# Performance work log

Measured on AMD Instinct MI355X. Metric: run time of the kernel, lower is better.

The kernel has to match this reference:

```python
import jax, jax.numpy as jnp
import numpy as np

N_EMBED = 256
N_HEADS = 4
HEAD_SIZE = N_EMBED // N_HEADS  # 64
BLOCK_SIZE = 768
LN_EPS = 1e-5


def layer_norm(x, g, b):
    mu = jnp.mean(x, axis=-1, keepdims=True)
    var = jnp.var(x, axis=-1, keepdims=True)
    return (x - mu) * jax.lax.rsqrt(var + LN_EPS) * g + b


def setup_inputs() -> dict:
    key = jax.random.key(0)
    ks = jax.random.split(key, 12)
    B, T, C, H, hs = 32, BLOCK_SIZE, N_EMBED, N_HEADS, HEAD_SIZE
    s_in = 1.0 / np.sqrt(C)
    s_ff = 1.0 / np.sqrt(4 * C)
    return {
        "x": jax.random.normal(ks[0], (B, T, C), jnp.float32),
        # per-head projections, stacked: [H, C, hs]
        "Wq": jax.random.normal(ks[1], (H, C, hs), jnp.float32) * s_in,
        "Wk": jax.random.normal(ks[2], (H, C, hs), jnp.float32) * s_in,
        "Wv": jax.random.normal(ks[3], (H, C, hs), jnp.float32) * s_in,
        "Wo": jax.random.normal(ks[4], (C, C), jnp.float32) * s_in,
        "bo": jnp.zeros((C,), jnp.float32),
        "W1": jax.random.normal(ks[5], (C, 4 * C), jnp.float32) * s_in,
        "b1": jnp.zeros((4 * C,), jnp.float32),
        "W2": jax.random.normal(ks[6], (4 * C, C), jnp.float32) * s_ff,
        "b2": jnp.zeros((C,), jnp.float32),
        "g1": jnp.ones((C,), jnp.float32),
        "be1": jnp.zeros((C,), jnp.float32),
        "g2": jnp.ones((C,), jnp.float32),
        "be2": jnp.zeros((C,), jnp.float32),
    }


def reference(x, Wq, Wk, Wv, Wo, bo, W1, b1, W2, b2, g1, be1, g2, be2):
    B, T, C = x.shape
    # --- multi-head causal self-attention (pre-LN) ---
    h = layer_norm(x, g1, be1)
    q = jnp.einsum("btc,hcd->bhtd", h, Wq)
    k = jnp.einsum("btc,hcd->bhtd", h, Wk)
    v = jnp.einsum("btc,hcd->bhtd", h, Wv)
    scores = jnp.einsum("bhtd,bhsd->bhts", q, k) * (HEAD_SIZE ** -0.5)
    causal = jnp.tril(jnp.ones((T, T), bool))
    scores = jnp.where(causal, scores, -jnp.inf)
    attn = jax.nn.softmax(scores, axis=-1)  # dropout = identity (eval)
    o = jnp.einsum("bhts,bhsd->bhtd", attn, v)
    o = o.transpose(0, 2, 1, 3).reshape(B, T, C)  # concat heads
    x = x + o @ Wo + bo
    # --- feed-forward (pre-LN) ---
    h2 = layer_norm(x, g2, be2)
    x = x + jax.nn.relu(h2 @ W1 + b1) @ W2 + b2
    return x
```

## Files before the change

kernel.cpp:

```cpp
#include <hip/hip_runtime.h>
#include <stdint.h>

using short8   = __attribute__((ext_vector_type(8))) short;
using f32x4    = __attribute__((ext_vector_type(4))) float;
using ushort4v = __attribute__((ext_vector_type(4))) unsigned short;
using uint2v   = __attribute__((ext_vector_type(2))) unsigned int;

#define CSC  0.1803368801111f
#define FIXC 20.0f

__device__ __forceinline__ unsigned short f2bf(float f) {
    unsigned int u = __builtin_bit_cast(unsigned int, f);
    u += 0x7FFFu + ((u >> 16) & 1u);
    return (unsigned short)(u >> 16);
}
__device__ __forceinline__ float bf2f(unsigned short s) {
    unsigned int u = ((unsigned int)s) << 16;
    return __builtin_bit_cast(float, u);
}
__device__ __forceinline__ unsigned pk2bf(float a, float b) {
    unsigned r;
    asm("v_cvt_pk_bf16_f32 %0, %1, %2" : "=v"(r) : "v"(a), "v"(b));
    return r;
}

__device__ __forceinline__ void gload16(const void* g, void* l) {
    __builtin_amdgcn_global_load_lds(
        (const __attribute__((address_space(1))) void*)(uintptr_t)g,
        (__attribute__((address_space(3))) void*)(unsigned)(uintptr_t)l,
        16, 0, 0);
}

__device__ __forceinline__ uint2v ln_row_pk(f32x4 v, f32x4 gv, f32x4 bvv) {
    float s  = v[0] + v[1] + v[2] + v[3];
    float s2 = v[0]*v[0] + v[1]*v[1] + v[2]*v[2] + v[3]*v[3];
    for (int m = 1; m < 64; m <<= 1) {
        s  += __shfl_xor(s,  m, 64);
        s2 += __shfl_xor(s2, m, 64);
    }
    float mu  = s * (1.0f / 256.0f);
    float var = s2 * (1.0f / 256.0f) - mu * mu;
    float rs  = rsqrtf(var + 1e-5f);
    float r0 = (v[0] - mu) * rs * gv[0] + bvv[0];
    float r1 = (v[1] - mu) * rs * gv[1] + bvv[1];
    float r2 = (v[2] - mu) * rs * gv[2] + bvv[2];
    float r3 = (v[3] - mu) * rs * gv[3] + bvv[3];
    uint2v u; u[0] = pk2bf(r0, r1); u[1] = pk2bf(r2, r3);
    return u;
}

__global__ __launch_bounds__(256) void prep_k(const float* __restrict__ x, const float* __restrict__ g1,
                                              const float* __restrict__ be1, unsigned short* __restrict__ h,
                                              const float* __restrict__ Wq, const float* __restrict__ Wk,
                                              const float* __restrict__ Wv, const float* __restrict__ Wo,
                                              const float* __restrict__ W1, const float* __restrict__ W2,
                                              unsigned short* __restrict__ wpackT, unsigned short* __restrict__ woT,
                                              unsigned short* __restrict__ w1T, unsigned short* __restrict__ w2T) {
    __shared__ float t[64][65];
    if (blockIdx.x >= 192) {
        int row  = (blockIdx.x - 192) * 4 + (threadIdx.x >> 6);
        int lane = threadIdx.x & 63;
        f32x4 v = *(const f32x4*)(x + (size_t)row * 256 + lane * 4);
        f32x4 gv = *(const f32x4*)(g1 + lane * 4);
        f32x4 bv = *(const f32x4*)(be1 + lane * 4);
        uint2v u = ln_row_pk(v, gv, bv);
        *(uint2v*)(h + (size_t)row * 256 + lane * 4) = u;
        return;
    }
    const int bid = blockIdx.x;
    const float* in; unsigned short* out;
    int R, C, r0, c0;
    if (bid < 48) {
        int z = bid >> 2, cx = bid & 3;
        int qkv = z >> 2, hh = z & 3;
        in = ((qkv == 0) ? Wq : (qkv == 1) ? Wk : Wv) + (size_t)hh * 256 * 64;
        out = wpackT + (size_t)(qkv * 256 + hh * 64) * 256;
        R = 256; C = 64; r0 = cx * 64; c0 = 0;
    } else if (bid < 64) {
        int tt = bid - 48;
        in = Wo; out = woT; R = 256; C = 256; r0 = (tt >> 2) * 64; c0 = (tt & 3) * 64;
    } else if (bid < 128) {
        int tt = bid - 64;
        in = W1; out = w1T; R = 256; C = 1024; r0 = (tt & 3) * 64; c0 = (tt >> 2) * 64;
    } else {
        int tt = bid - 128;
        in = W2; out = w2T; R = 1024; C = 256; r0 = (tt & 15) * 64; c0 = (tt >> 4) * 64;
    }
    const int tx = threadIdx.x & 63, ty = threadIdx.x >> 6;
    #pragma unroll
    for (int i = 0; i < 64; i += 4)
        t[i + ty][tx] = in[(size_t)(r0 + i + ty) * C + c0 + tx];
    __syncthreads();
    #pragma unroll
    for (int i = 0; i < 64; i += 4)
        out[(size_t)(c0 + i + ty) * R + r0 + tx] = f2bf(t[tx][i + ty]);
}

__global__ __launch_bounds__(256) void qkv_k(const unsigned short* __restrict__ h,
                                             const unsigned short* __restrict__ wpackT,
                                             unsigned short* __restrict__ qk,
                                             unsigned short* __restrict__ vT) {
    __shared__ unsigned short As[128 * 64];
    __shared__ unsigned short Bs[128 * 64];
    const int tid  = threadIdx.x;
    const int lane = tid & 63;
    const int w    = tid >> 6;
    const int wm   = w >> 1, wn = w & 1;
    const int l15  = lane & 15, l4 = lane >> 4;
    const int bid  = blockIdx.x;

    const unsigned short *A, *BT;
    unsigned short* outp;
    int bm, bn, N;
    float qsc = 1.0f;
    if (bid < 768) {
        bn = bid & 3;  bm = bid >> 2;
        A = h; BT = wpackT; outp = qk; N = 512;
        if (bn < 2) qsc = CSC;
    } else {
        int t = bid - 768;
        bm = t & 1;    bn = t >> 1;
        A = wpackT + 512 * 256; BT = h; outp = vT; N = 24576;
    }
    const int K = 256;

    f32x4 acc[4][4] = {};

    const size_t K2 = (size_t)K * 2;
    const int i0   = w * 4096 + lane * 16;
    const int row0 = i0 >> 7;
    const int cb0  = (i0 & 127) ^ ((row0 & 7) << 4);
    const char* aSrc = (const char*)A  + ((size_t)(bm * 128 + row0)) * K2 + cb0;
    const char* bSrc = (const char*)BT + ((size_t)(bn * 128 + row0)) * K2 + cb0;

    for (int t = 0; t < 4; ++t) {
        {
            const char* aS = aSrc + (size_t)t * 128;
            const char* bS = bSrc + (size_t)t * 128;
            char* aD = (char*)&As[0] + w * 4096;
            char* bD = (char*)&Bs[0] + w * 4096;
            #pragma unroll
            for (int c = 0; c < 4; ++c) {
                gload16(aS + (size_t)c * 8 * K2, aD + c * 1024);
                gload16(bS + (size_t)c * 8 * K2, bD + c * 1024);
            }
        }
        __syncthreads();
        #pragma unroll
        for (int kf = 0; kf < 2; ++kf) {
            int kb = kf * 64 + l4 * 16;
            short8 af[4], bfr[4];
            #pragma unroll
            for (int mf = 0; mf < 4; ++mf) {
                int row = wm * 64 + mf * 16 + l15;
                af[mf] = *(const short8*)((const char*)&As[0] + ((row * 128 + kb) ^ ((row & 7) << 4)));
            }
            #pragma unroll
            for (int nf = 0; nf < 4; ++nf) {
                int row = wn * 64 + nf * 16 + l15;
                bfr[nf] = *(const short8*)((const char*)&Bs[0] + ((row * 128 + kb) ^ ((row & 7) << 4)));
            }
            #pragma unroll
            for (int mf = 0; mf < 4; ++mf)
                #pragma unroll
                for (int nf = 0; nf < 4; ++nf)
                    acc[mf][nf] = __builtin_amdgcn_mfma_f32_16x16x32_bf16(af[mf], bfr[nf], acc[mf][nf], 0, 0, 0);
        }
        __syncthreads();
    }

    #pragma unroll
    for (int nf = 0; nf < 4; ++nf) {
        int col = bn * 128 + wn * 64 + nf * 16 + l15;
        #pragma unroll
        for (int mf = 0; mf < 4; ++mf) {
            int row0o = bm * 128 + wm * 64 + mf * 16 + l4 * 4;
            size_t off = (size_t)row0o * N + col;
            unsigned p01 = pk2bf(acc[mf][nf][0] * qsc, acc[mf][nf][1] * qsc);
            unsigned p23 = pk2bf(acc[mf][nf][2] * qsc, acc[mf][nf][3] * qsc);
            outp[off]                 = (unsigned short)p01;
            outp[off + (size_t)N]     = (unsigned short)(p01 >> 16);
            outp[off + (size_t)N * 2] = (unsigned short)p23;
            outp[off + (size_t)N * 3] = (unsigned short)(p23 >> 16);
        }
    }
}

template <int EPI, bool DB>
__global__ __launch_bounds__(256) void gemm_bt(const unsigned short* __restrict__ A,
                                               const unsigned short* __restrict__ BT,
                                               void* __restrict__ outp,
                                               const float* __restrict__ bias,
                                               const void* __restrict__ resid,
                                               int K, int N) {
    __shared__ unsigned short As[DB ? 2 : 1][128 * 64];
    __shared__ unsigned short Bs[DB ? 2 : 1][128 * 64];
    const int tid  = threadIdx.x;
    const int lane = tid & 63;
    const int w    = tid >> 6;
    const int wm   = w >> 1, wn = w & 1;
    const int bm   = blockIdx.y, bn = blockIdx.x;
    const int l15  = lane & 15, l4 = lane >> 4;

    f32x4 acc[4][4] = {};

    const size_t K2 = (size_t)K * 2;
    const int i0   = w * 4096 + lane * 16;
    const int row0 = i0 >> 7;
    const int cb0  = (i0 & 127) ^ ((row0 & 7) << 4);
    const char* aSrc = (const char*)A  + ((size_t)(bm * 128 + row0)) * K2 + cb0;
    const char* bSrc = (const char*)BT + ((size_t)(bn * 128 + row0)) * K2 + cb0;
    const int nt = K >> 6;

    auto stage = [&](int t, int buf) {
        const char* aS = aSrc + (size_t)t * 128;
        const char* bS = bSrc + (size_t)t * 128;
        char* aD = (char*)&As[buf][0] + w * 4096;
        char* bD = (char*)&Bs[buf][0] + w * 4096;
        #pragma unroll
        for (int c = 0; c < 4; ++c) {
            gload16(aS + (size_t)c * 8 * K2, aD + c * 1024);
            gload16(bS + (size_t)c * 8 * K2, bD + c * 1024);
        }
    };
    auto compute = [&](int buf) {
        const char* AsB = (const char*)&As[buf][0];
        const char* BsB = (const char*)&Bs[buf][0];
        #pragma unroll
        for (int kf = 0; kf < 2; ++kf) {
            int kb = kf * 64 + l4 * 16;
            short8 af[4], bfr[4];
            #pragma unroll
            for (int mf = 0; mf < 4; ++mf) {
                int row = wm * 64 + mf * 16 + l15;
                af[mf] = *(const short8*)(AsB + ((row * 128 + kb) ^ ((row & 7) << 4)));
            }
            #pragma unroll
            for (int nf = 0; nf < 4; ++nf) {
                int row = wn * 64 + nf * 16 + l15;
                bfr[nf] = *(const short8*)(BsB + ((row * 128 + kb) ^ ((row & 7) << 4)));
            }
            #pragma unroll
            for (int mf = 0; mf < 4; ++mf)
                #pragma unroll
                for (int nf = 0; nf < 4; ++nf)
                    acc[mf][nf] = __builtin_amdgcn_mfma_f32_16x16x32_bf16(af[mf], bfr[nf], acc[mf][nf], 0, 0, 0);
        }
    };

    if (DB) {
        stage(0, 0);
        for (int t = 0; t < nt; ++t) {
            const int cur = t & 1;
            __syncthreads();
            if (t + 1 < nt) stage(t + 1, cur ^ 1);
            compute(cur);
        }
    } else {
        for (int t = 0; t < nt; ++t) {
            stage(t, 0);
            __syncthreads();
            compute(0);
            __syncthreads();
        }
    }

    #pragma unroll
    for (int nf = 0; nf < 4; ++nf) {
        int col = bn * 128 + wn * 64 + nf * 16 + l15;
        float bv = bias[col];
        #pragma unroll
        for (int mf = 0; mf < 4; ++mf) {
            int row0o = bm * 128 + wm * 64 + mf * 16 + l4 * 4;
            size_t off = (size_t)row0o * N + col;
            float v[4];
            #pragma unroll
            for (int r = 0; r < 4; ++r)
                v[r] = acc[mf][nf][r] + bv + ((const float*)resid)[off + (size_t)r * N];
            unsigned short* O = (unsigned short*)outp;
            unsigned p01 = pk2bf(v[0], v[1]), p23 = pk2bf(v[2], v[3]);
            O[off]                 = (unsigned short)p01;
            O[off + (size_t)N]     = (unsigned short)(p01 >> 16);
            O[off + (size_t)N * 2] = (unsigned short)p23;
            O[off + (size_t)N * 3] = (unsigned short)(p23 >> 16);
        }
    }
}

__global__ __launch_bounds__(256) void ff_fused(const unsigned short* __restrict__ x1b,
                                                const float* __restrict__ g2,
                                                const float* __restrict__ be2,
                                                const unsigned short* __restrict__ w1T,
                                                const unsigned short* __restrict__ w2T,
                                                const float* __restrict__ b1,
                                                const float* __restrict__ b2,
                                                float* __restrict__ out) {
    __shared__ unsigned short sA[4][32 * 64];
    __shared__ unsigned short sW[16384];
    __shared__ unsigned short sAct[32 * 64];
    const int tid = threadIdx.x, lane = tid & 63, w = tid >> 6;
    const int l15 = lane & 15, l4 = lane >> 4;
    const int wm = w >> 1, wn = w & 1;
    const int r0 = blockIdx.x * 32;

    {
        f32x4 gv = *(const f32x4*)(g2 + lane * 4);
        f32x4 bv = *(const f32x4*)(be2 + lane * 4);
        const int ks = lane >> 4, colb = (lane & 15) * 8;
        #pragma unroll
        for (int it = 0; it < 8; ++it) {
            int row = it * 4 + w;
            ushort4v u4 = *(const ushort4v*)(x1b + (size_t)(r0 + row) * 256 + lane * 4);
            f32x4 v;
            #pragma unroll
            for (int i = 0; i < 4; ++i) v[i] = bf2f(u4[i]);
            uint2v u = ln_row_pk(v, gv, bv);
            *(uint2v*)((char*)&sA[0][0] + ks * 4096 + row * 128 + (colb ^ ((row & 7) << 4))) = u;
        }
    }

    f32x4 oacc[8] = {};

    for (int c = 0; c < 16; ++c) {
        {
            const char* wb = (const char*)w1T + (size_t)(c * 64) * 512;
            #pragma unroll
            for (int g = 0; g < 8; ++g) {
                int j = g * 4096 + tid * 16;
                int ks = j >> 13, row = (j >> 7) & 63, cb = j & 127;
                gload16(wb + (size_t)row * 512 + ks * 128 + (cb ^ ((row & 7) << 4)),
                        (char*)&sW[0] + j);
            }
        }
        __syncthreads();

        f32x4 aacc[2] = {};
        __builtin_amdgcn_s_setprio(1);
        #pragma unroll
        for (int ks = 0; ks < 4; ++ks) {
            #pragma unroll
            for (int kf = 0; kf < 2; ++kf) {
                const int kb = kf * 64 + l4 * 16;
                int hrow = wm * 16 + l15;
                short8 hf = *(const short8*)((const char*)&sA[ks][0] + ((hrow * 128 + kb) ^ ((hrow & 7) << 4)));
                #pragma unroll
                for (int nf = 0; nf < 2; ++nf) {
                    int row = wn * 32 + nf * 16 + l15;
                    short8 wf = *(const short8*)((const char*)&sW[ks * 4096] + ((row * 128 + kb) ^ ((row & 7) << 4)));
                    aacc[nf] = __builtin_amdgcn_mfma_f32_16x16x32_bf16(wf, hf, aacc[nf], 0, 0, 0);
                }
            }
        }
        __builtin_amdgcn_s_setprio(0);
        #pragma unroll
        for (int nf = 0; nf < 2; ++nf) {
            int nl = wn * 32 + nf * 16 + l4 * 4;
            f32x4 bv = *(const f32x4*)(b1 + c * 64 + nl);
            float v0 = aacc[nf][0] + bv[0]; v0 = v0 > 0.0f ? v0 : 0.0f;
            float v1 = aacc[nf][1] + bv[1]; v1 = v1 > 0.0f ? v1 : 0.0f;
            float v2 = aacc[nf][2] + bv[2]; v2 = v2 > 0.0f ? v2 : 0.0f;
            float v3 = aacc[nf][3] + bv[3]; v3 = v3 > 0.0f ? v3 : 0.0f;
            uint2v u; u[0] = pk2bf(v0, v1); u[1] = pk2bf(v2, v3);
            int m = wm * 16 + l15;
            *(uint2v*)((char*)&sAct[0] + ((m * 128 + nl * 2) ^ ((m & 7) << 4))) = u;
        }
        __syncthreads();

        {
            const char* wb = (const char*)w2T + (size_t)c * 128;
            #pragma unroll
            for (int g = 0; g < 8; ++g) {
                int j = g * 4096 + tid * 16;
                int row = j >> 7, cb = j & 127;
                gload16(wb + (size_t)row * 2048 + (cb ^ ((row & 7) << 4)),
                        (char*)&sW[0] + j);
            }
        }
        __syncthreads();

        __builtin_amdgcn_s_setprio(1);
        #pragma unroll
        for (int kf = 0; kf < 2; ++kf) {
            const int kb = kf * 64 + l4 * 16;
            int arow = wm * 16 + l15;
            short8 af = *(const short8*)((const char*)&sAct[0] + ((arow * 128 + kb) ^ ((arow & 7) << 4)));
            #pragma unroll
            for (int nf = 0; nf < 8; ++nf) {
                int row = wn * 128 + nf * 16 + l15;
                short8 wf = *(const short8*)((const char*)&sW[0] + ((row * 128 + kb) ^ ((row & 7) << 4)));
                oacc[nf] = __builtin_amdgcn_mfma_f32_16x16x32_bf16(af, wf, oacc[nf], 0, 0, 0);
            }
        }
        __builtin_amdgcn_s_setprio(0);
        __syncthreads();
    }

    #pragma unroll
    for (int nf = 0; nf < 8; ++nf) {
        const int col = wn * 128 + nf * 16 + l15;
        const float bv = b2[col];
        const int row = r0 + wm * 16 + l4 * 4;
        const size_t off = (size_t)row * 256 + col;
        #pragma unroll
        for (int r = 0; r < 4; ++r)
            out[off + (size_t)r * 256] = oacc[nf][r] + bv + bf2f(x1b[off + (size_t)r * 256]);
    }
}

__global__ __launch_bounds__(256) void attn_k(const unsigned short* __restrict__ qk,
                                              const unsigned short* __restrict__ vT,
                                              unsigned short* __restrict__ o) {
    __shared__ unsigned short Ks[2][64 * 64];
    __shared__ unsigned short Vt[2][64 * 64];
    __shared__ unsigned short Pl[4][16 * 64];
    const int tid = threadIdx.x, lane = tid & 63, w = tid >> 6;
    const int l15 = lane & 15, l4 = lane >> 4;
    const int gid = blockIdx.x;
    const int xcd = gid & 7, slot = gid >> 3;
    const int sl6 = slot / 6;
    const int bh  = xcd * 16 + sl6;
    const int x   = slot - sl6 * 6;
    const int qb1 = x, qb2 = 11 - x;
    const int b = bh >> 2, h = bh & 3;
    const unsigned short* Qb = qk + (size_t)b * 768 * 512 + h * 64;
    const char* Kg = (const char*)(Qb + 256);
    const char* Vg = (const char*)(vT + (size_t)(h * 64) * 24576 + (size_t)b * 768);
    const int t01 = qb1 * 64, t02 = qb2 * 64;
    const int tq1 = t01 + w * 16 + l15;
    const int tq2 = t02 + w * 16 + l15;

    short8 q1f0 = *(const short8*)(Qb + (size_t)tq1 * 512 + l4 * 8);
    short8 q1f1 = *(const short8*)(Qb + (size_t)tq1 * 512 + 32 + l4 * 8);
    short8 q2f0 = *(const short8*)(Qb + (size_t)tq2 * 512 + l4 * 8);
    short8 q2f1 = *(const short8*)(Qb + (size_t)tq2 * 512 + 32 + l4 * 8);

    const int srow = w * 16 + (lane >> 3);
    const int scb  = ((lane & 7) * 16) ^ ((srow & 7) << 4);
    const char* kSrc = Kg + (size_t)srow * 1024 + scb;
    const char* vSrc = Vg + (size_t)srow * 49152 + scb;
    char* kDst0 = (char*)&Ks[0][0] + w * 2048;
    char* vDst0 = (char*)&Vt[0][0] + w * 2048;

    f32x4 oA[4] = {}, oB[4] = {};
    float lsA = 0.0f, lsB = 0.0f;
    unsigned short* Pw = &Pl[w][0];
    const char* KsB;
    const char* VtB;
    int sb = 0;

    auto do_tile = [&](short8 qf0, short8 qf1, f32x4 (&oacc)[4], float& lsum, bool diag, int tq) {
        f32x4 sacc[4] = {};
        __builtin_amdgcn_s_setprio(1);
        #pragma unroll
        for (int kf = 0; kf < 2; ++kf) {
            const int kb = kf * 64 + l4 * 16;
            short8 qf = kf ? qf1 : qf0;
            #pragma unroll
            for (int nf = 0; nf < 4; ++nf) {
                int sr = nf * 16 + l15;
                short8 kfr = *(const short8*)(KsB + ((sr * 128 + kb) ^ ((sr & 7) << 4)));
                sacc[nf] = __builtin_amdgcn_mfma_f32_16x16x32_bf16(kfr, qf, sacc[nf], 0, 0, 0);
            }
        }
        __builtin_amdgcn_s_setprio(0);

        if (diag) {
            #pragma unroll
            for (int nf = 0; nf < 4; ++nf)
                #pragma unroll
                for (int r = 0; r < 4; ++r) {
                    int s = sb * 64 + nf * 16 + l4 * 4 + r;
                    if (s > tq) sacc[nf][r] = -1e30f;
                }
        }
        float psum = 0.0f;
        #pragma unroll
        for (int nf = 0; nf < 4; ++nf) {
            float p0 = __builtin_amdgcn_exp2f(sacc[nf][0] - FIXC);
            float p1 = __builtin_amdgcn_exp2f(sacc[nf][1] - FIXC);
            float p2 = __builtin_amdgcn_exp2f(sacc[nf][2] - FIXC);
            float p3 = __builtin_amdgcn_exp2f(sacc[nf][3] - FIXC);
            psum += (p0 + p1) + (p2 + p3);
            uint2v u; u[0] = pk2bf(p0, p1); u[1] = pk2bf(p2, p3);
            *(uint2v*)((char*)Pw + ((l15 * 128 + nf * 32 + l4 * 8) ^ ((l15 & 7) << 4))) = u;
        }
        psum += __shfl_xor(psum, 16, 64);
        psum += __shfl_xor(psum, 32, 64);
        lsum += psum;

        __builtin_amdgcn_s_setprio(1);
        #pragma unroll
        for (int kf = 0; kf < 2; ++kf) {
            const int kb = kf * 64 + l4 * 16;
            short8 pa = *(const short8*)((const char*)Pw + ((l15 * 128 + kb) ^ ((l15 & 7) << 4)));
            #pragma unroll
            for (int nf = 0; nf < 4; ++nf) {
                int dr = nf * 16 + l15;
                short8 vfr = *(const short8*)(VtB + ((dr * 128 + kb) ^ ((dr & 7) << 4)));
                oacc[nf] = __builtin_amdgcn_mfma_f32_16x16x32_bf16(pa, vfr, oacc[nf], 0, 0, 0);
            }
        }
        __builtin_amdgcn_s_setprio(0);
    };

    gload16(kSrc, kDst0);                 gload16(kSrc + 8 * 1024, kDst0 + 1024);
    gload16(vSrc, vDst0);                 gload16(vSrc + 8 * 49152, vDst0 + 1024);

    for (sb = 0; sb <= qb2; ++sb) {
        const int pb = sb & 1;
        __syncthreads();
        if (sb < qb2) {
            const char* ks = kSrc + (size_t)(sb + 1) * 65536;
            const char* vs = vSrc + (size_t)(sb + 1) * 128;
            char* kd = kDst0 + (pb ^ 1) * 8192;
            char* vd = vDst0 + (pb ^ 1) * 8192;
            gload16(ks, kd);              gload16(ks + 8 * 1024, kd + 1024);
            gload16(vs, vd);              gload16(vs + 8 * 49152, vd + 1024);
        }
        KsB = (const char*)&Ks[0][0] + pb * 8192;
        VtB = (const char*)&Vt[0][0] + pb * 8192;

        do_tile(q2f0, q2f1, oB, lsB, sb == qb2, tq2);
        if (sb <= qb1) do_tile(q1f0, q1f1, oA, lsA, sb == qb1, tq1);
    }

    float liA = 1.0f / lsA, liB = 1.0f / lsB;
    float lrA[4], lrB[4];
    #pragma unroll
    for (int r = 0; r < 4; ++r) {
        lrA[r] = __shfl(liA, l4 * 4 + r, 64);
        lrB[r] = __shfl(liB, l4 * 4 + r, 64);
    }
    const int tA = t01 + w * 16 + l4 * 4;
    const int tB = t02 + w * 16 + l4 * 4;
    unsigned short* oa = o + ((size_t)(b * 768 + tA)) * 256 + h * 64;
    unsigned short* ob = o + ((size_t)(b * 768 + tB)) * 256 + h * 64;
    #pragma unroll
    for (int nf = 0; nf < 4; ++nf) {
        unsigned a01 = pk2bf(oA[nf][0] * lrA[0], oA[nf][1] * lrA[1]);
        unsigned a23 = pk2bf(oA[nf][2] * lrA[2], oA[nf][3] * lrA[3]);
        unsigned b01 = pk2bf(oB[nf][0] * lrB[0], oB[nf][1] * lrB[1]);
        unsigned b23 = pk2bf(oB[nf][2] * lrB[2], oB[nf][3] * lrB[3]);
        oa[nf * 16 + l15]       = (unsigned short)a01;
        oa[256 + nf * 16 + l15] = (unsigned short)(a01 >> 16);
        oa[512 + nf * 16 + l15] = (unsigned short)a23;
        oa[768 + nf * 16 + l15] = (unsigned short)(a23 >> 16);
        ob[nf * 16 + l15]       = (unsigned short)b01;
        ob[256 + nf * 16 + l15] = (unsigned short)(b01 >> 16);
        ob[512 + nf * 16 + l15] = (unsigned short)b23;
        ob[768 + nf * 16 + l15] = (unsigned short)(b23 >> 16);
    }
}

extern "C" void kernel_launch(void* const* d_in, const int* in_sizes, int n_in,
                              void* d_out, int out_size, void* d_ws, size_t ws_size,
                              hipStream_t stream) {
    const float* x   = (const float*)d_in[0];
    const float* Wq  = (const float*)d_in[1];
    const float* Wk  = (const float*)d_in[2];
    const float* Wv  = (const float*)d_in[3];
    const float* Wo  = (const float*)d_in[4];
    const float* bo  = (const float*)d_in[5];
    const float* W1  = (const float*)d_in[6];
    const float* b1  = (const float*)d_in[7];
    const float* W2  = (const float*)d_in[8];
    const float* b2  = (const float*)d_in[9];
    const float* g1  = (const float*)d_in[10];
    const float* be1 = (const float*)d_in[11];
    const float* g2  = (const float*)d_in[12];
    const float* be2 = (const float*)d_in[13];

    char* ws = (char*)d_ws;
    unsigned short* qk_ws  = (unsigned short*)(ws + 0);
    unsigned short* vT_ws  = (unsigned short*)(ws + 25165824);
    unsigned short* o_ws   = (unsigned short*)(ws + 37748736);
    unsigned short* h_ws   = (unsigned short*)(ws + 50331648);
    unsigned short* x1b_ws = (unsigned short*)(ws + 62914560);
    unsigned short* wpackT = (unsigned short*)(ws + 88080384);
    unsigned short* woT    = (unsigned short*)(ws + 88473600);
    unsigned short* w1T    = (unsigned short*)(ws + 88604672);
    unsigned short* w2T    = (unsigned short*)(ws + 89128960);

    prep_k<<<6336, 256, 0, stream>>>(x, g1, be1, h_ws, Wq, Wk, Wv, Wo, W1, W2, wpackT, woT, w1T, w2T);
    qkv_k<<<1152, 256, 0, stream>>>(h_ws, wpackT, qk_ws, vT_ws);
    attn_k<<<768, 256, 0, stream>>>(qk_ws, vT_ws, o_ws);
    gemm_bt<2, true><<<dim3(2, 192), 256, 0, stream>>>(o_ws, woT, x1b_ws, bo, x, 256, 256);
    ff_fused<<<768, 256, 0, stream>>>(x1b_ws, g2, be2, w1T, w2T, b1, b2, (float*)d_out);
}
```

Baseline: 121.1 us.

## Split fused feed-forward into tiled FF1 kernel and generic GEMM, remap blocks per XCD

Replaces the fused feed-forward kernel, which streamed W1/W2 chunks for each 32-row tile, with two kernels. The first is a 128x128-tiled LN+W1+ReLU kernel that writes bf16 activations to workspace. The second reuses the existing gemm_bt with a new epilogue that adds bias and the bf16 residual and writes fp32 output. Block indices in qkv_k and ff1_k are remapped so neighbouring row tiles land on the same XCD for better L2 reuse. The split lowers repeated weight reloads and raises MFMA reuse, but adds a 48MB bf16 activation round trip through memory and one more launch.

```diff
diff --git a/kernel.cpp b/kernel.cpp
--- a/kernel.cpp
+++ b/kernel.cpp
@@ -114,12 +114,16 @@
     int bm, bn, N;
     float qsc = 1.0f;
     if (bid < 768) {
-        bn = bid & 3;  bm = bid >> 2;
+        const int xcd = bid & 7, i = bid >> 3;
+        bm = xcd * 24 + (i >> 2);
+        bn = i & 3;
         A = h; BT = wpackT; outp = qk; N = 512;
         if (bn < 2) qsc = CSC;
     } else {
-        int t = bid - 768;
-        bm = t & 1;    bn = t >> 1;
+        const int t = bid - 768;
+        const int xcd = t & 7, j = t >> 3;
+        bn = xcd * 24 + (j >> 1);
+        bm = j & 1;
         A = wpackT + 512 * 256; BT = h; outp = vT; N = 24576;
     }
     const int K = 256;
@@ -275,135 +279,116 @@
             size_t off = (size_t)row0o * N + col;
             float v[4];
             #pragma unroll
-            for (int r = 0; r < 4; ++r)
-                v[r] = acc[mf][nf][r] + bv + ((const float*)resid)[off + (size_t)r * N];
-            unsigned short* O = (unsigned short*)outp;
-            unsigned p01 = pk2bf(v[0], v[1]), p23 = pk2bf(v[2], v[3]);
-            O[off]                 = (unsigned short)p01;
-            O[off + (size_t)N]     = (unsigned short)(p01 >> 16);
-            O[off + (size_t)N * 2] = (unsigned short)p23;
-            O[off + (size_t)N * 3] = (unsigned short)(p23 >> 16);
-        }
-    }
-}
-
-__global__ __launch_bounds__(256) void ff_fused(const unsigned short* __restrict__ x1b,
-                                                const float* __restrict__ g2,
-                                                const float* __restrict__ be2,
-                                                const unsigned short* __restrict__ w1T,
-                                                const unsigned short* __restrict__ w2T,
-                                                const float* __restrict__ b1,
-                                                const float* __restrict__ b2,
-                                                float* __restrict__ out) {
-    __shared__ unsigned short sA[4][32 * 64];
-    __shared__ unsigned short sW[16384];
-    __shared__ unsigned short sAct[32 * 64];
+            for (int r = 0; r < 4; ++r) {
+                v[r] = acc[mf][nf][r] + bv;
+                if (EPI == 2) v[r] += ((const float*)resid)[off + (size_t)r * N];
+            }
+            if (EPI == 4) {
+                #pragma unroll
+                for (int r = 0; r < 4; ++r)
+                    ((float*)outp)[off + (size_t)r * N] =
+                        v[r] + bf2f(((const unsigned short*)resid)[off + (size_t)r * N]);
+            } else {
+                unsigned short* O = (unsigned short*)outp;
+                unsigned p01 = pk2bf(v[0], v[1]), p23 = pk2bf(v[2], v[3]);
+                O[off]                 = (unsigned short)p01;
+                O[off + (size_t)N]     = (unsigned short)(p01 >> 16);
+                O[off + (size_t)N * 2] = (unsigned short)p23;
+                O[off + (size_t)N * 3] = (unsigned short)(p23 >> 16);
+            }
+        }
+    }
+}
+
+__global__ __launch_bounds__(256) void ff1_k(const unsigned short* __restrict__ x1b,
+                                             const float* __restrict__ g2,
+                                             const float* __restrict__ be2,
+                                             const unsigned short* __restrict__ w1T,
+                                             const float* __restrict__ b1,
+                                             unsigned short* __restrict__ a_out) {
+    __shared__ unsigned short sA[4][128 * 64];
+    __shared__ unsigned short sB[128 * 64];
     const int tid = threadIdx.x, lane = tid & 63, w = tid >> 6;
     const int l15 = lane & 15, l4 = lane >> 4;
     const int wm = w >> 1, wn = w & 1;
-    const int r0 = blockIdx.x * 32;
+    const int bid = blockIdx.x;
+    const int xcd = bid & 7, i = bid >> 3;
+    const int bm = xcd * 24 + (i >> 3);
+    const int bn = i & 7;
+    const int r0 = bm * 128;
 
     {
         f32x4 gv = *(const f32x4*)(g2 + lane * 4);
         f32x4 bv = *(const f32x4*)(be2 + lane * 4);
         const int ks = lane >> 4, colb = (lane & 15) * 8;
         #pragma unroll
-        for (int it = 0; it < 8; ++it) {
+        for (int it = 0; it < 32; ++it) {
             int row = it * 4 + w;
             ushort4v u4 = *(const ushort4v*)(x1b + (size_t)(r0 + row) * 256 + lane * 4);
             f32x4 v;
             #pragma unroll
-            for (int i = 0; i < 4; ++i) v[i] = bf2f(u4[i]);
+            for (int q = 0; q < 4; ++q) v[q] = bf2f(u4[q]);
             uint2v u = ln_row_pk(v, gv, bv);
-            *(uint2v*)((char*)&sA[0][0] + ks * 4096 + row * 128 + (colb ^ ((row & 7) << 4))) = u;
-        }
-    }
-
-    f32x4 oacc[8] = {};
-
-    for (int c = 0; c < 16; ++c) {
+            *(uint2v*)((char*)&sA[0][0] + ks * 16384 + row * 128 + (colb ^ ((row & 7) << 4))) = u;
+        }
+    }
+
+    f32x4 acc[4][4] = {};
+
+    for (int t = 0; t < 4; ++t) {
         {
-            const char* wb = (const char*)w1T + (size_t)(c * 64) * 512;
-            #pragma unroll
-            for (int g = 0; g < 8; ++g) {
-                int j = g * 4096 + tid * 16;
-                int ks = j >> 13, row = (j >> 7) & 63, cb = j & 127;
-                gload16(wb + (size_t)row * 512 + ks * 128 + (cb ^ ((row & 7) << 4)),
-                        (char*)&sW[0] + j);
-            }
-        }
-        __syncthreads();
-
-        f32x4 aacc[2] = {};
-        __builtin_amdgcn_s_setprio(1);
-        #pragma unroll
-        for (int ks = 0; ks < 4; ++ks) {
-            #pragma unroll
-            for (int kf = 0; kf < 2; ++kf) {
-                const int kb = kf * 64 + l4 * 16;
-                int hrow = wm * 16 + l15;
-                short8 hf = *(const short8*)((const char*)&sA[ks][0] + ((hrow * 128 + kb) ^ ((hrow & 7) << 4)));
-                #pragma unroll
-                for (int nf = 0; nf < 2; ++nf) {
-                    int row = wn * 32 + nf * 16 + l15;
-                    short8 wf = *(const short8*)((const char*)&sW[ks * 4096] + ((row * 128 + kb) ^ ((row & 7) << 4)));
-                    aacc[nf] = __builtin_amdgcn_mfma_f32_16x16x32_bf16(wf, hf, aacc[nf], 0, 0, 0);
-                }
-            }
-        }
-        __builtin_amdgcn_s_setprio(0);
-        #pragma unroll
-        for (int nf = 0; nf < 2; ++nf) {
-            int nl = wn * 32 + nf * 16 + l4 * 4;
-            f32x4 bv = *(const f32x4*)(b1 + c * 64 + nl);
-            float v0 = aacc[nf][0] + bv[0]; v0 = v0 > 0.0f ? v0 : 0.0f;
-            float v1 = aacc[nf][1] + bv[1]; v1 = v1 > 0.0f ? v1 : 0.0f;
-            float v2 = aacc[nf][2] + bv[2]; v2 = v2 > 0.0f ? v2 : 0.0f;
-            float v3 = aacc[nf][3] + bv[3]; v3 = v3 > 0.0f ? v3 : 0.0f;
-            uint2v u; u[0] = pk2bf(v0, v1); u[1] = pk2bf(v2, v3);
-            int m = wm * 16 + l15;
-            *(uint2v*)((char*)&sAct[0] + ((m * 128 + nl * 2) ^ ((m & 7) << 4))) = u;
-        }
-        __syncthreads();
-
-        {
-            const char* wb = (const char*)w2T + (size_t)c * 128;
-            #pragma unroll
-            for (int g = 0; g < 8; ++g) {
+            const char* wb = (const char*)w1T + (size_t)(bn * 128) * 512 + t * 128;
+            #pragma unroll
+            for (int g = 0; g < 4; ++g) {
                 int j = g * 4096 + tid * 16;
                 int row = j >> 7, cb = j & 127;
-                gload16(wb + (size_t)row * 2048 + (cb ^ ((row & 7) << 4)),
-                        (char*)&sW[0] + j);
+                gload16(wb + (size_t)row * 512 + (cb ^ ((row & 7) << 4)),
+                        (char*)&sB[0] + j);
             }
         }
         __syncthreads();
-
-        __builtin_amdgcn_s_setprio(1);
         #pragma unroll
         for (int kf = 0; kf < 2; ++kf) {
-            const int kb = kf * 64 + l4 * 16;
-            int arow = wm * 16 + l15;
-            short8 af = *(const short8*)((const char*)&sAct[0] + ((arow * 128 + kb) ^ ((arow & 7) << 4)));
-            #pragma unroll
-            for (int nf = 0; nf < 8; ++nf) {
-                int row = wn * 128 + nf * 16 + l15;
-                short8 wf = *(const short8*)((const char*)&sW[0] + ((row * 128 + kb) ^ ((row & 7) << 4)));
-                oacc[nf] = __builtin_amdgcn_mfma_f32_16x16x32_bf16(af, wf, oacc[nf], 0, 0, 0);
-            }
-        }
-        __builtin_amdgcn_s_setprio(0);
+            int kb = kf * 64 + l4 * 16;
+            short8 af[4], bfr[4];
+            #pragma unroll
+            for (int mf = 0; mf < 4; ++mf) {
+                int row = wm * 64 + mf * 16 + l15;
+                af[mf] = *(const short8*)((const char*)&sA[0][0] + t * 16384
+                           + ((row * 128 + kb) ^ ((row & 7) << 4)));
+            }
+            #pragma unroll
+            for (int nf = 0; nf < 4; ++nf) {
+                int row = wn * 64 + nf * 16 + l15;
+                bfr[nf] = *(const short8*)((const char*)&sB[0] + ((row * 128 + kb) ^ ((row & 7) << 4)));
+            }
+            #pragma unroll
+            for (int mf = 0; mf < 4; ++mf)
+                #pragma unroll
+                for (int nf = 0; nf < 4; ++nf)
+                    acc[mf][nf] = __builtin_amdgcn_mfma_f32_16x16x32_bf16(af[mf], bfr[nf], acc[mf][nf], 0, 0, 0);
+        }
         __syncthreads();
     }
 
     #pragma unroll
-    for (int nf = 0; nf < 8; ++nf) {
-        const int col = wn * 128 + nf * 16 + l15;
-        const float bv = b2[col];
-        const int row = r0 + wm * 16 + l4 * 4;
-        const size_t off = (size_t)row * 256 + col;
-        #pragma unroll
-        for (int r = 0; r < 4; ++r)
-            out[off + (size_t)r * 256] = oacc[nf][r] + bv + bf2f(x1b[off + (size_t)r * 256]);
+    for (int nf = 0; nf < 4; ++nf) {
+        int col = bn * 128 + wn * 64 + nf * 16 + l15;
+        float bv = b1[col];
+        #pragma unroll
+        for (int mf = 0; mf < 4; ++mf) {
+            int row0o = r0 + wm * 64 + mf * 16 + l4 * 4;
+            size_t off = (size_t)row0o * 1024 + col;
+            float v0 = acc[mf][nf][0] + bv; v0 = v0 > 0.0f ? v0 : 0.0f;
+            float v1 = acc[mf][nf][1] + bv; v1 = v1 > 0.0f ? v1 : 0.0f;
+            float v2 = acc[mf][nf][2] + bv; v2 = v2 > 0.0f ? v2 : 0.0f;
+            float v3 = acc[mf][nf][3] + bv; v3 = v3 > 0.0f ? v3 : 0.0f;
+            unsigned p01 = pk2bf(v0, v1), p23 = pk2bf(v2, v3);
+            a_out[off]        = (unsigned short)p01;
+            a_out[off + 1024] = (unsigned short)(p01 >> 16);
+            a_out[off + 2048] = (unsigned short)p23;
+            a_out[off + 3072] = (unsigned short)(p23 >> 16);
+        }
     }
 }
 
@@ -574,6 +559,7 @@
     unsigned short* qk_ws  = (unsigned short*)(ws + 0);
     unsigned short* vT_ws  = (unsigned short*)(ws + 25165824);
     unsigned short* o_ws   = (unsigned short*)(ws + 37748736);
+    unsigned short* a_ws   = (unsigned short*)(ws + 0);
     unsigned short* h_ws   = (unsigned short*)(ws + 50331648);
     unsigned short* x1b_ws = (unsigned short*)(ws + 62914560);
     unsigned short* wpackT = (unsigned short*)(ws + 88080384);
@@ -585,5 +571,6 @@
     qkv_k<<<1152, 256, 0, stream>>>(h_ws, wpackT, qk_ws, vT_ws);
     attn_k<<<768, 256, 0, stream>>>(qk_ws, vT_ws, o_ws);
     gemm_bt<2, true><<<dim3(2, 192), 256, 0, stream>>>(o_ws, woT, x1b_ws, bo, x, 256, 256);
-    ff_fused<<<768, 256, 0, stream>>>(x1b_ws, g2, be2, w1T, w2T, b1, b2, (float*)d_out);
-}
+    ff1_k<<<1536, 256, 0, stream>>>(x1b_ws, g2, be2, w1T, b1, a_ws);
+    gemm_bt<4, true><<<dim3(2, 192), 256, 0, stream>>>(a_ws, w2T, d_out, b2, x1b_ws, 1024, 256);
+}
```

New measurement: 140.2 us. 15.8% more time.
